# Kernel optimization log

Measured on AMD Instinct MI355X. Metric: run time of the kernel, lower is better.

## Reference

```python
import jax, jax.numpy as jnp
import numpy as np

N, E, C_IN, C_OUT, K = 50000, 800000, 64, 64, 3

def setup_inputs() -> dict:
    key = jax.random.key(0)
    k1, k2, k3, k4, k5, k6 = jax.random.split(key, 6)
    x = jax.random.normal(k1, (N, C_IN), dtype=jnp.float32)
    row = jax.random.randint(k2, (E,), 0, N)
    col = jax.random.randint(k3, (E,), 0, N)
    # PyG ChebConv removes self loops; avoid generating them
    col = jnp.where(col == row, (col + 1) % N, col)
    edge_index = jnp.stack([row, col])
    edge_weight = jax.random.uniform(k4, (E,), dtype=jnp.float32)
    # ChebConv learned params: one [C_in, C_out] matrix per Chebyshev order, plus bias
    W = jax.random.normal(k5, (K, C_IN, C_OUT), dtype=jnp.float32) / np.sqrt(C_IN).astype(np.float32)
    b = jax.random.normal(k6, (C_OUT,), dtype=jnp.float32) * 0.01
    return {"x": x, "edge_index": edge_index, "edge_weight": edge_weight, "W": W, "b": b}


def reference(x, edge_index, edge_weight, W, b):
    row, col = edge_index[0], edge_index[1]
    # PyG ChebConv.__norm__ with sym normalization and lambda_max = 2.0:
    # L_hat = (2/lambda_max) * (I - D^{-1/2} A D^{-1/2}) - I = -D^{-1/2} A D^{-1/2}
    deg = jax.ops.segment_sum(edge_weight, row, num_segments=N)
    dis = jnp.where(deg > 0, jax.lax.rsqrt(deg), 0.0)  # deg_inv_sqrt, inf -> 0
    w = -dis[row] * edge_weight * dis[col]             # [E] normalized Laplacian weights

    def prop(h):  # sparse matvec: L_hat @ h, [N, C]
        return jax.ops.segment_sum(w[:, None] * h[col], row, num_segments=N)

    # Chebyshev recurrence: T0 = x, T1 = L_hat x, Tk = 2 L_hat T_{k-1} - T_{k-2}
    Tx0 = x
    out = Tx0 @ W[0]
    Tx1 = prop(Tx0)
    out = out + Tx1 @ W[1]
    for k in range(2, K):
        Tx2 = 2.0 * prop(Tx1) - Tx0
        out = out + Tx2 @ W[k]
        Tx0, Tx1 = Tx1, Tx2
    return jax.nn.relu(out + b)
```

## Files before the change

kernel.cpp:

```cpp
#include <hip/hip_runtime.h>
#include <hip/hip_bf16.h>

#define C 64
#define NCOPY 8
#define FXSCALE 16777216.0f
#define LOW44 ((1ULL << 44) - 1)

typedef unsigned short u16;

__device__ __forceinline__ u16 f2bf_rne(float v) {
    unsigned u = __float_as_uint(v);
    u += 0x7FFFu + ((u >> 16) & 1u);
    return (u16)(u >> 16);
}
__device__ __forceinline__ float bf2f(u16 u) {
    return __uint_as_float((unsigned)u << 16);
}

__global__ __launch_bounds__(256) void hist8_kernel(const int* __restrict__ row,
                                                    const float* __restrict__ ew,
                                                    unsigned long long* __restrict__ cd8,
                                                    u16* __restrict__ rank16,
                                                    int E, int N) {
    int t = threadIdx.x;
    int base = blockIdx.x * 1024;
    int copy = blockIdx.x & (NCOPY - 1);
    size_t cb = (size_t)copy * N;

    unsigned long long old[4];
    int e[4];
#pragma unroll
    for (int u = 0; u < 4; u++) {
        e[u] = base + u * 256 + t;
        if (e[u] < E) {
            int r = row[e[u]];
            unsigned long long fx = (unsigned long long)__float2uint_rn(ew[e[u]] * FXSCALE);
            unsigned long long inc = (1ULL << 44) | fx;
            old[u] = atomicAdd(&cd8[cb + r], inc);
        }
    }
#pragma unroll
    for (int u = 0; u < 4; u++) {
        if (e[u] < E) rank16[e[u]] = (u16)(old[u] >> 44);
    }
}

__global__ __launch_bounds__(256) void scanA_kernel(const unsigned long long* __restrict__ cd8,
                                                    int* __restrict__ cnt,
                                                    float* __restrict__ dis,
                                                    int* __restrict__ bsum, int N) {
    __shared__ int s[256];
    int t = threadIdx.x;
    int i = blockIdx.x * 256 + t;
    int cv = 0;
    unsigned long long dfx = 0;
    if (i < N) {
#pragma unroll
        for (int c = 0; c < NCOPY; c++) {
            unsigned long long v = cd8[(size_t)c * N + i];
            cv += (int)(v >> 44);
            dfx += (v & LOW44);
        }
        cnt[i] = cv;
        float dv = (float)dfx * (1.0f / FXSCALE);
        dis[i] = (dv > 0.0f) ? rsqrtf(dv) : 0.0f;
    }
    s[t] = cv;
    __syncthreads();
    for (int off = 128; off > 0; off >>= 1) {
        if (t < off) s[t] += s[t + off];
        __syncthreads();
    }
    if (t == 0) bsum[blockIdx.x] = s[0];
}

__global__ __launch_bounds__(256) void scanB_kernel(int* __restrict__ bsum,
                                                    int* __restrict__ rowptr,
                                                    int G, int N) {
    __shared__ int s[256];
    int t = threadIdx.x;
    int v = (t < G) ? bsum[t] : 0;
    s[t] = v;
    __syncthreads();
    for (int off = 1; off < 256; off <<= 1) {
        int u = (t >= off) ? s[t - off] : 0;
        __syncthreads();
        s[t] += u;
        __syncthreads();
    }
    if (t < G) bsum[t] = s[t] - v;
    if (t == 255) rowptr[N] = s[255];
}

__global__ __launch_bounds__(256) void scanC_kernel(const int* __restrict__ cnt,
                                                    const unsigned long long* __restrict__ cd8,
                                                    int* __restrict__ start8,
                                                    const int* __restrict__ bsum,
                                                    int* __restrict__ rowptr,
                                                    const float* __restrict__ dis,
                                                    const float* __restrict__ x,
                                                    u16* __restrict__ xg,
                                                    int N) {
    __shared__ int s[256];
    __shared__ float sdis[256];
    int t = threadIdx.x;
    int i = blockIdx.x * 256 + t;
    int v = (i < N) ? cnt[i] : 0;
    if (i < N) sdis[t] = dis[i];
    s[t] = v;
    __syncthreads();
    for (int off = 1; off < 256; off <<= 1) {
        int u = (t >= off) ? s[t - off] : 0;
        __syncthreads();
        s[t] += u;
        __syncthreads();
    }
    if (i < N) {
        int rp = bsum[blockIdx.x] + s[t] - v;
        rowptr[i] = rp;
        int run = rp;
#pragma unroll
        for (int c = 0; c < NCOPY; c++) {
            int tmp = (int)(cd8[(size_t)c * N + i] >> 44);
            start8[(size_t)c * N + i] = run;
            run += tmp;
        }
    }
    size_t nb = (size_t)blockIdx.x * 16384;
#pragma unroll 1
    for (int it = 0; it < 16; it++) {
        int idx4 = it * 256 + t;
        int lr = idx4 >> 4;
        int gr = blockIdx.x * 256 + lr;
        if (gr < N) {
            float4 vv = *(const float4*)(x + nb + (size_t)idx4 * 4);
            float di = sdis[lr];
            ushort4 o;
            o.x = f2bf_rne(vv.x * di); o.y = f2bf_rne(vv.y * di);
            o.z = f2bf_rne(vv.z * di); o.w = f2bf_rne(vv.w * di);
            *(ushort4*)(xg + nb + (size_t)idx4 * 4) = o;
        }
    }
}

__global__ __launch_bounds__(256) void scatter_kernel(const int* __restrict__ row,
                                                      const int* __restrict__ col,
                                                      const float* __restrict__ ew,
                                                      const int* __restrict__ start8,
                                                      const u16* __restrict__ rank16,
                                                      unsigned* __restrict__ epk,
                                                      int E, int N) {
    int t = threadIdx.x;
    int base = blockIdx.x * 1024;
    int copy = blockIdx.x & (NCOPY - 1);
    size_t cb = (size_t)copy * N;
#pragma unroll
    for (int u = 0; u < 4; u++) {
        int e = base + u * 256 + t;
        if (e < E) {
            int r = row[e];
            unsigned pk = ((unsigned)col[e] << 16) | (unsigned)f2bf_rne(ew[e]);
            int pos = start8[cb + r] + (int)rank16[e];
            epk[pos] = pk;
        }
    }
}

__global__ __launch_bounds__(256) void spmm_csr_kernel(
        const int* __restrict__ rowptr,
        const unsigned* __restrict__ epk,
        const float* __restrict__ dis,
        const unsigned* __restrict__ h32,
        float* __restrict__ out32,
        unsigned* __restrict__ outbf,
        int N, int writebf) {
    int wid = (blockIdx.x * blockDim.x + threadIdx.x) >> 6;
    int lane = threadIdx.x & 63;
    if (wid >= N) return;
    int half = lane >> 5;
    int cp   = lane & 31;
    int beg = rowptr[wid];
    int end = rowptr[wid + 1];
    float ax0 = 0.f, ay0 = 0.f, ax1 = 0.f, ay1 = 0.f;
    float ax2 = 0.f, ay2 = 0.f, ax3 = 0.f, ay3 = 0.f;
    for (int base = beg; base < end; base += 64) {
        int idx = base + lane;
        unsigned ed = (idx < end) ? epk[idx] : 0u;
        int cnt = end - base; if (cnt > 64) cnt = 64;
        for (int j = 0; j < cnt; j += 8) {
            unsigned e0 = (unsigned)__shfl((int)ed, j + half);
            unsigned e1 = (unsigned)__shfl((int)ed, j + 2 + half);
            unsigned e2 = (unsigned)__shfl((int)ed, j + 4 + half);
            unsigned e3 = (unsigned)__shfl((int)ed, j + 6 + half);
            float w0 = bf2f((u16)(e0 & 0xffffu)); int c0 = (int)(e0 >> 16);
            float w1 = bf2f((u16)(e1 & 0xffffu)); int c1 = (int)(e1 >> 16);
            float w2 = bf2f((u16)(e2 & 0xffffu)); int c2 = (int)(e2 >> 16);
            float w3 = bf2f((u16)(e3 & 0xffffu)); int c3 = (int)(e3 >> 16);
            unsigned hv0 = h32[(size_t)c0 * 32 + cp];
            unsigned hv1 = h32[(size_t)c1 * 32 + cp];
            unsigned hv2 = h32[(size_t)c2 * 32 + cp];
            unsigned hv3 = h32[(size_t)c3 * 32 + cp];
            ax0 = fmaf(w0, bf2f((u16)(hv0 & 0xffffu)), ax0);
            ay0 = fmaf(w0, bf2f((u16)(hv0 >> 16)),     ay0);
            ax1 = fmaf(w1, bf2f((u16)(hv1 & 0xffffu)), ax1);
            ay1 = fmaf(w1, bf2f((u16)(hv1 >> 16)),     ay1);
            ax2 = fmaf(w2, bf2f((u16)(hv2 & 0xffffu)), ax2);
            ay2 = fmaf(w2, bf2f((u16)(hv2 >> 16)),     ay2);
            ax3 = fmaf(w3, bf2f((u16)(hv3 & 0xffffu)), ax3);
            ay3 = fmaf(w3, bf2f((u16)(hv3 >> 16)),     ay3);
        }
    }
    float ax = (ax0 + ax1) + (ax2 + ax3);
    float ay = (ay0 + ay1) + (ay2 + ay3);
    float bx = __shfl(ax, cp + 32);
    float by = __shfl(ay, cp + 32);
    if (half == 0) {
        float dr = dis[wid];
        float rx = -dr * (ax + bx);
        float ry = -dr * (ay + by);
        *(float2*)(out32 + (size_t)wid * C + 2 * cp) = make_float2(rx, ry);
        if (writebf) {
            unsigned pk = (unsigned)f2bf_rne(dr * rx) | ((unsigned)f2bf_rne(dr * ry) << 16);
            outbf[(size_t)wid * 32 + cp] = pk;
        }
    }
}

__global__ __launch_bounds__(256) void final_gemm_kernel(
        const float* __restrict__ x,
        const float* __restrict__ T1,
        const float* __restrict__ P,
        const float* __restrict__ W,
        const float* __restrict__ b,
        float* __restrict__ out, int N) {
    __shared__ float As[16][64];
    __shared__ float Ws[16][64];

    int t  = threadIdx.x;
    int tx = t & 15;
    int ty = t >> 4;
    int n0 = blockIdx.x * 64;

    int sn = t >> 2;
    int skb = (t & 3) * 4;

    float acc[4][4];
#pragma unroll
    for (int i = 0; i < 4; i++)
#pragma unroll
        for (int j = 0; j < 4; j++) acc[i][j] = 0.0f;

#pragma unroll 1
    for (int s = 0; s < 12; s++) {
        float4 wv = *(const float4*)(W + s * 1024 + t * 4);
        int nn = n0 + sn;
        float4 av = make_float4(0.f, 0.f, 0.f, 0.f);
        if (nn < N) {
            if (s < 4) {
                av = *(const float4*)(x + (size_t)nn * C + s * 16 + skb);
            } else if (s < 8) {
                av = *(const float4*)(T1 + (size_t)nn * C + (s - 4) * 16 + skb);
            } else {
                float4 pv = *(const float4*)(P + (size_t)nn * C + (s - 8) * 16 + skb);
                float4 xv = *(const float4*)(x + (size_t)nn * C + (s - 8) * 16 + skb);
                av = make_float4(2.0f * pv.x - xv.x, 2.0f * pv.y - xv.y,
                                 2.0f * pv.z - xv.z, 2.0f * pv.w - xv.w);
            }
        }
        __syncthreads();
        {
            int wk = (t * 4) >> 6;
            int wc = (t * 4) & 63;
            *(float4*)&Ws[wk][wc] = wv;
        }
        As[skb + 0][sn] = av.x;
        As[skb + 1][sn] = av.y;
        As[skb + 2][sn] = av.z;
        As[skb + 3][sn] = av.w;
        __syncthreads();

#pragma unroll
        for (int kk = 0; kk < 16; kk++) {
            float4 a4 = *(const float4*)&As[kk][ty * 4];
            float4 w4 = *(const float4*)&Ws[kk][tx * 4];
            float ar[4] = {a4.x, a4.y, a4.z, a4.w};
            float wr[4] = {w4.x, w4.y, w4.z, w4.w};
#pragma unroll
            for (int i = 0; i < 4; i++)
#pragma unroll
                for (int j = 0; j < 4; j++)
                    acc[i][j] = fmaf(ar[i], wr[j], acc[i][j]);
        }
    }

    float4 bv = *(const float4*)(b + tx * 4);
    float br[4] = {bv.x, bv.y, bv.z, bv.w};
#pragma unroll
    for (int i = 0; i < 4; i++) {
        int node = n0 + ty * 4 + i;
        if (node < N) {
            float4 o;
            o.x = fmaxf(acc[i][0] + br[0], 0.0f);
            o.y = fmaxf(acc[i][1] + br[1], 0.0f);
            o.z = fmaxf(acc[i][2] + br[2], 0.0f);
            o.w = fmaxf(acc[i][3] + br[3], 0.0f);
            *(float4*)(out + (size_t)node * C + tx * 4) = o;
        }
    }
}

extern "C" void kernel_launch(void* const* d_in, const int* in_sizes, int n_in,
                              void* d_out, int out_size, void* d_ws, size_t ws_size,
                              hipStream_t stream) {
    const float* x  = (const float*)d_in[0];
    const int*   ei = (const int*)d_in[1];
    const float* ew = (const float*)d_in[2];
    const float* W  = (const float*)d_in[3];
    const float* b  = (const float*)d_in[4];
    float* out = (float*)d_out;

    const int N = in_sizes[0] / C;
    const int E = in_sizes[2];
    const int* row = ei;
    const int* col = ei + E;

    char* ws = (char*)d_ws;
    size_t off = 0;
    auto alloc = [&](size_t bytes) {
        void* p = ws + off;
        off = (off + bytes + 255) & ~(size_t)255;
        return p;
    };
    float*    dis    = (float*)alloc((size_t)N * 4);
    int*      cnt    = (int*)alloc((size_t)N * 4);
    int*      rowptr = (int*)alloc((size_t)(N + 1) * 4);
    unsigned* epk    = (unsigned*)alloc((size_t)E * 4);
    float*    T1     = (float*)alloc((size_t)N * C * 4);
    float*    P      = (float*)alloc((size_t)N * C * 4);
    int*      bsum   = (int*)alloc((size_t)256 * 4);
    unsigned long long* cd8 = (unsigned long long*)alloc((size_t)NCOPY * N * 8);
    int*      start8 = (int*)alloc((size_t)NCOPY * N * 4);
    u16*      rank16 = (u16*)alloc((size_t)E * 2);
    u16*      xg     = (u16*)alloc((size_t)N * C * 2);
    u16*      T1g    = (u16*)alloc((size_t)N * C * 2);

    hipMemsetAsync(cd8, 0, (size_t)NCOPY * N * 8, stream);

    const int B = 256;
    const int G = (N + B - 1) / B;

    int histBlocks = (E + 1023) / 1024;
    hist8_kernel<<<histBlocks, B, 0, stream>>>(row, ew, cd8, rank16, E, N);
    scanA_kernel<<<G, B, 0, stream>>>(cd8, cnt, dis, bsum, N);
    scanB_kernel<<<1, B, 0, stream>>>(bsum, rowptr, G, N);
    scanC_kernel<<<G, B, 0, stream>>>(cnt, cd8, start8, bsum, rowptr,
                                      dis, x, xg, N);
    scatter_kernel<<<histBlocks, B, 0, stream>>>(row, col, ew, start8,
                                                 rank16, epk, E, N);

    int spmm_blocks = (int)(((long long)N * 64 + B - 1) / B);
    spmm_csr_kernel<<<spmm_blocks, B, 0, stream>>>(rowptr, epk, dis,
                                                   (const unsigned*)xg,
                                                   T1, (unsigned*)T1g, N, 1);
    spmm_csr_kernel<<<spmm_blocks, B, 0, stream>>>(rowptr, epk, dis,
                                                   (const unsigned*)T1g,
                                                   P, (unsigned*)T1g, N, 0);

    final_gemm_kernel<<<(N + 63) / 64, B, 0, stream>>>(x, T1, P, W, b, out, N);
}
```

Before: 205.7 us.

## Fuse CSR-building frontend into one persistent kernel with grid barriers

Replaces the five separate preprocessing kernels (histogram, three scan stages, scatter) with a single persistent 256-block kernel that uses atomic-counter grid barriers between phases. It also drops the 8-way replicated degree counters in favour of a single counter array, which simplifies the start-offset computation. The aim is to remove launch overhead and inter-kernel gaps. In exchange it raises atomic contention on the shared counters, relies on all 256 blocks being co-resident for the spin barrier, and runs the grid-stride loops on fewer threads.

```diff
diff --git a/kernel.cpp b/kernel.cpp
--- a/kernel.cpp
+++ b/kernel.cpp
@@ -2,9 +2,10 @@
 #include <hip/hip_bf16.h>
 
 #define C 64
-#define NCOPY 8
 #define FXSCALE 16777216.0f
 #define LOW44 ((1ULL << 44) - 1)
+#define FGRID 256
+#define FT (FGRID * 256)
 
 typedef unsigned short u16;
 
@@ -17,152 +18,109 @@
     return __uint_as_float((unsigned)u << 16);
 }
 
-__global__ __launch_bounds__(256) void hist8_kernel(const int* __restrict__ row,
-                                                    const float* __restrict__ ew,
-                                                    unsigned long long* __restrict__ cd8,
-                                                    u16* __restrict__ rank16,
-                                                    int E, int N) {
-    int t = threadIdx.x;
-    int base = blockIdx.x * 1024;
-    int copy = blockIdx.x & (NCOPY - 1);
-    size_t cb = (size_t)copy * N;
-
-    unsigned long long old[4];
-    int e[4];
-#pragma unroll
-    for (int u = 0; u < 4; u++) {
-        e[u] = base + u * 256 + t;
-        if (e[u] < E) {
-            int r = row[e[u]];
-            unsigned long long fx = (unsigned long long)__float2uint_rn(ew[e[u]] * FXSCALE);
-            unsigned long long inc = (1ULL << 44) | fx;
-            old[u] = atomicAdd(&cd8[cb + r], inc);
-        }
-    }
-#pragma unroll
-    for (int u = 0; u < 4; u++) {
-        if (e[u] < E) rank16[e[u]] = (u16)(old[u] >> 44);
-    }
-}
-
-__global__ __launch_bounds__(256) void scanA_kernel(const unsigned long long* __restrict__ cd8,
-                                                    int* __restrict__ cnt,
-                                                    float* __restrict__ dis,
-                                                    int* __restrict__ bsum, int N) {
+__device__ __forceinline__ void gridbar(int* cnt, int target) {
+    __syncthreads();
+    if (threadIdx.x == 0) {
+        __threadfence();
+        atomicAdd(cnt, 1);
+        while (atomicAdd(cnt, 0) < target) {
+            __builtin_amdgcn_s_sleep(2);
+        }
+        __threadfence();
+    }
+    __syncthreads();
+}
+
+__global__ __launch_bounds__(256) void frontend_kernel(
+        const float* __restrict__ x,
+        const int* __restrict__ row,
+        const int* __restrict__ col,
+        const float* __restrict__ ew,
+        int* __restrict__ barcnt,
+        unsigned long long* __restrict__ cd,
+        int* __restrict__ rowptr,
+        int* __restrict__ bsum,
+        u16* __restrict__ rank16,
+        unsigned* __restrict__ epk,
+        float* __restrict__ dis,
+        u16* __restrict__ xg,
+        int E, int N) {
     __shared__ int s[256];
     int t = threadIdx.x;
-    int i = blockIdx.x * 256 + t;
-    int cv = 0;
-    unsigned long long dfx = 0;
-    if (i < N) {
-#pragma unroll
-        for (int c = 0; c < NCOPY; c++) {
-            unsigned long long v = cd8[(size_t)c * N + i];
-            cv += (int)(v >> 44);
-            dfx += (v & LOW44);
-        }
-        cnt[i] = cv;
-        float dv = (float)dfx * (1.0f / FXSCALE);
-        dis[i] = (dv > 0.0f) ? rsqrtf(dv) : 0.0f;
-    }
-    s[t] = cv;
-    __syncthreads();
-    for (int off = 128; off > 0; off >>= 1) {
-        if (t < off) s[t] += s[t + off];
-        __syncthreads();
-    }
-    if (t == 0) bsum[blockIdx.x] = s[0];
-}
-
-__global__ __launch_bounds__(256) void scanB_kernel(int* __restrict__ bsum,
-                                                    int* __restrict__ rowptr,
-                                                    int G, int N) {
-    __shared__ int s[256];
-    int t = threadIdx.x;
-    int v = (t < G) ? bsum[t] : 0;
-    s[t] = v;
-    __syncthreads();
-    for (int off = 1; off < 256; off <<= 1) {
-        int u = (t >= off) ? s[t - off] : 0;
-        __syncthreads();
-        s[t] += u;
-        __syncthreads();
-    }
-    if (t < G) bsum[t] = s[t] - v;
-    if (t == 255) rowptr[N] = s[255];
-}
-
-__global__ __launch_bounds__(256) void scanC_kernel(const int* __restrict__ cnt,
-                                                    const unsigned long long* __restrict__ cd8,
-                                                    int* __restrict__ start8,
-                                                    const int* __restrict__ bsum,
-                                                    int* __restrict__ rowptr,
-                                                    const float* __restrict__ dis,
-                                                    const float* __restrict__ x,
-                                                    u16* __restrict__ xg,
-                                                    int N) {
-    __shared__ int s[256];
-    __shared__ float sdis[256];
-    int t = threadIdx.x;
-    int i = blockIdx.x * 256 + t;
-    int v = (i < N) ? cnt[i] : 0;
-    if (i < N) sdis[t] = dis[i];
-    s[t] = v;
-    __syncthreads();
-    for (int off = 1; off < 256; off <<= 1) {
-        int u = (t >= off) ? s[t - off] : 0;
-        __syncthreads();
-        s[t] += u;
-        __syncthreads();
-    }
-    if (i < N) {
-        int rp = bsum[blockIdx.x] + s[t] - v;
-        rowptr[i] = rp;
-        int run = rp;
-#pragma unroll
-        for (int c = 0; c < NCOPY; c++) {
-            int tmp = (int)(cd8[(size_t)c * N + i] >> 44);
-            start8[(size_t)c * N + i] = run;
-            run += tmp;
-        }
-    }
-    size_t nb = (size_t)blockIdx.x * 16384;
-#pragma unroll 1
-    for (int it = 0; it < 16; it++) {
-        int idx4 = it * 256 + t;
-        int lr = idx4 >> 4;
-        int gr = blockIdx.x * 256 + lr;
-        if (gr < N) {
-            float4 vv = *(const float4*)(x + nb + (size_t)idx4 * 4);
-            float di = sdis[lr];
-            ushort4 o;
-            o.x = f2bf_rne(vv.x * di); o.y = f2bf_rne(vv.y * di);
-            o.z = f2bf_rne(vv.z * di); o.w = f2bf_rne(vv.w * di);
-            *(ushort4*)(xg + nb + (size_t)idx4 * 4) = o;
-        }
-    }
-}
-
-__global__ __launch_bounds__(256) void scatter_kernel(const int* __restrict__ row,
-                                                      const int* __restrict__ col,
-                                                      const float* __restrict__ ew,
-                                                      const int* __restrict__ start8,
-                                                      const u16* __restrict__ rank16,
-                                                      unsigned* __restrict__ epk,
-                                                      int E, int N) {
-    int t = threadIdx.x;
-    int base = blockIdx.x * 1024;
-    int copy = blockIdx.x & (NCOPY - 1);
-    size_t cb = (size_t)copy * N;
-#pragma unroll
-    for (int u = 0; u < 4; u++) {
-        int e = base + u * 256 + t;
-        if (e < E) {
-            int r = row[e];
-            unsigned pk = ((unsigned)col[e] << 16) | (unsigned)f2bf_rne(ew[e]);
-            int pos = start8[cb + r] + (int)rank16[e];
-            epk[pos] = pk;
-        }
+    int bid = blockIdx.x;
+    int gtid = bid * 256 + t;
+    const int G = (N + 255) / 256;
+
+    for (int e = gtid; e < E; e += FT) {
+        int r = row[e];
+        unsigned long long fx = (unsigned long long)__float2uint_rn(ew[e] * FXSCALE);
+        unsigned long long old = atomicAdd(&cd[r], (1ULL << 44) | fx);
+        rank16[e] = (u16)(old >> 44);
+    }
+    gridbar(barcnt, 1 * FGRID);
+
+    if (bid < G) {
+        int i = bid * 256 + t;
+        int cv = 0;
+        if (i < N) {
+            unsigned long long v = cd[i];
+            cv = (int)(v >> 44);
+            float dv = (float)(v & LOW44) * (1.0f / FXSCALE);
+            dis[i] = (dv > 0.0f) ? rsqrtf(dv) : 0.0f;
+        }
+        s[t] = cv;
+        __syncthreads();
+        for (int o = 128; o > 0; o >>= 1) {
+            if (t < o) s[t] += s[t + o];
+            __syncthreads();
+        }
+        if (t == 0) bsum[bid] = s[0];
+    }
+    gridbar(barcnt, 2 * FGRID);
+
+    if (bid == 0) {
+        int v = (t < G) ? bsum[t] : 0;
+        s[t] = v;
+        __syncthreads();
+        for (int o = 1; o < 256; o <<= 1) {
+            int u = (t >= o) ? s[t - o] : 0;
+            __syncthreads();
+            s[t] += u;
+            __syncthreads();
+        }
+        if (t < G) bsum[t] = s[t] - v;
+        if (t == 255) rowptr[N] = s[255];
+    }
+    gridbar(barcnt, 3 * FGRID);
+
+    if (bid < G) {
+        int i = bid * 256 + t;
+        int v = (i < N) ? (int)(cd[i] >> 44) : 0;
+        s[t] = v;
+        __syncthreads();
+        for (int o = 1; o < 256; o <<= 1) {
+            int u = (t >= o) ? s[t - o] : 0;
+            __syncthreads();
+            s[t] += u;
+            __syncthreads();
+        }
+        if (i < N) rowptr[i] = bsum[bid] + s[t] - v;
+    }
+    for (int i4 = gtid; i4 < N * 16; i4 += FT) {
+        int r = i4 >> 4;
+        float di = dis[r];
+        float4 vv = *(const float4*)(x + (size_t)i4 * 4);
+        ushort4 o;
+        o.x = f2bf_rne(vv.x * di); o.y = f2bf_rne(vv.y * di);
+        o.z = f2bf_rne(vv.z * di); o.w = f2bf_rne(vv.w * di);
+        *(ushort4*)(xg + (size_t)i4 * 4) = o;
+    }
+    gridbar(barcnt, 4 * FGRID);
+
+    for (int e = gtid; e < E; e += FT) {
+        int r = row[e];
+        unsigned pk = ((unsigned)col[e] << 16) | (unsigned)f2bf_rne(ew[e]);
+        epk[rowptr[r] + (int)rank16[e]] = pk;
     }
 }
 
@@ -319,8 +277,8 @@
     const float* b  = (const float*)d_in[4];
     float* out = (float*)d_out;
 
-    const int N = in_sizes[0] / C;
-    const int E = in_sizes[2];
+    int N = in_sizes[0] / C;
+    int E = in_sizes[2];
     const int* row = ei;
     const int* col = ei + E;
 
@@ -331,33 +289,26 @@
         off = (off + bytes + 255) & ~(size_t)255;
         return p;
     };
+    int*      barcnt = (int*)alloc(4);
+    unsigned long long* cd = (unsigned long long*)alloc((size_t)N * 8);
+    size_t zero_bytes = off;
+    int*      rowptr = (int*)alloc((size_t)(N + 1) * 4);
+    int*      bsum   = (int*)alloc((size_t)256 * 4);
+    u16*      rank16 = (u16*)alloc((size_t)E * 2);
+    unsigned* epk    = (unsigned*)alloc((size_t)E * 4);
     float*    dis    = (float*)alloc((size_t)N * 4);
-    int*      cnt    = (int*)alloc((size_t)N * 4);
-    int*      rowptr = (int*)alloc((size_t)(N + 1) * 4);
-    unsigned* epk    = (unsigned*)alloc((size_t)E * 4);
     float*    T1     = (float*)alloc((size_t)N * C * 4);
     float*    P      = (float*)alloc((size_t)N * C * 4);
-    int*      bsum   = (int*)alloc((size_t)256 * 4);
-    unsigned long long* cd8 = (unsigned long long*)alloc((size_t)NCOPY * N * 8);
-    int*      start8 = (int*)alloc((size_t)NCOPY * N * 4);
-    u16*      rank16 = (u16*)alloc((size_t)E * 2);
     u16*      xg     = (u16*)alloc((size_t)N * C * 2);
     u16*      T1g    = (u16*)alloc((size_t)N * C * 2);
 
-    hipMemsetAsync(cd8, 0, (size_t)NCOPY * N * 8, stream);
+    hipMemsetAsync(ws, 0, zero_bytes, stream);
+
+    frontend_kernel<<<FGRID, 256, 0, stream>>>(x, row, col, ew, barcnt, cd,
+                                               rowptr, bsum, rank16, epk,
+                                               dis, xg, E, N);
 
     const int B = 256;
-    const int G = (N + B - 1) / B;
-
-    int histBlocks = (E + 1023) / 1024;
-    hist8_kernel<<<histBlocks, B, 0, stream>>>(row, ew, cd8, rank16, E, N);
-    scanA_kernel<<<G, B, 0, stream>>>(cd8, cnt, dis, bsum, N);
-    scanB_kernel<<<1, B, 0, stream>>>(bsum, rowptr, G, N);
-    scanC_kernel<<<G, B, 0, stream>>>(cnt, cd8, start8, bsum, rowptr,
-                                      dis, x, xg, N);
-    scatter_kernel<<<histBlocks, B, 0, stream>>>(row, col, ew, start8,
-                                                 rank16, epk, E, N);
-
     int spmm_blocks = (int)(((long long)N * 64 + B - 1) / B);
     spmm_csr_kernel<<<spmm_blocks, B, 0, stream>>>(rowptr, epk, dis,
                                                    (const unsigned*)xg,
```

Measured after the change: 277.8 us. +35.0%, slower.
